# Kernel tuning notes

Hardware: AMD Instinct MI355X
Metric: run time of the kernel (lower is better)

Reference implementation:

```python
import jax, jax.numpy as jnp
import numpy as np

N = 100000         # nodes
E = 800000         # directed edges (before self loops)
F_IN = 64          # num_node_features
HID = 128          # hidden_channels
HEADS = 4
HD = HID // HEADS  # head_dim = 32
NEG_SLOPE = 0.2    # GATv2Conv default negative_slope


def _layernorm(x, g, b, eps=1e-5):
    m = jnp.mean(x, axis=-1, keepdims=True)
    v = jnp.var(x, axis=-1, keepdims=True)
    return (x - m) * jax.lax.rsqrt(v + eps) * g + b


def _gatv2_conv(x, src, dst, w_l, w_r, att, heads, hd):
    # GATv2Conv (share_weights=False, bias=False, concat=True), inference mode.
    n = x.shape[0]
    x_l = (x @ w_l).reshape(n, heads, hd)   # source-side transform
    x_r = (x @ w_r).reshape(n, heads, hd)   # target-side transform
    x_j = x_l[src]                          # [Et, H, C] gather (messages)
    e = jax.nn.leaky_relu(x_j + x_r[dst], NEG_SLOPE)
    logits = jnp.einsum('ehc,hc->eh', e, att)            # [Et, H]
    m = jax.ops.segment_max(logits, dst, num_segments=n)  # stable segment softmax
    p = jnp.exp(logits - m[dst])
    s = jax.ops.segment_sum(p, dst, num_segments=n)
    alpha = p / s[dst]
    out = jax.ops.segment_sum(x_j * alpha[..., None], dst, num_segments=n)
    return out.reshape(n, heads * hd)


def _forward(edge_index, x, ln_in_g, ln_in_b, w_l1, w_r1, att1, ln1_g, ln1_b,
             w_l2, w_r2, att2, ln2_g, ln2_b, w_l3, w_r3, att3, ln3_g, ln3_b,
             rtt_w1, rtt_b1, rtt_w2, rtt_b2, ret_w1, ret_b1, ret_w2, ret_b2):
    n = x.shape[0]
    loops = jnp.arange(n, dtype=edge_index.dtype)
    src = jnp.concatenate([edge_index[0], loops])  # add_self_loops=True
    dst = jnp.concatenate([edge_index[1], loops])
    h = _layernorm(x, ln_in_g, ln_in_b)
    # layer 0: F_IN -> HID (4 heads), no residual (dims differ)
    h = _gatv2_conv(h, src, dst, w_l1, w_r1, att1, HEADS, HD)
    h = jax.nn.relu(_layernorm(h, ln1_g, ln1_b))
    # layer 1: HID -> HID (4 heads), residual * 0.1
    res = h
    h = _gatv2_conv(h, src, dst, w_l2, w_r2, att2, HEADS, HD)
    h = jax.nn.relu(_layernorm(h, ln2_g, ln2_b) + 0.1 * res)
    # layer 2: HID -> HID (1 head), residual * 0.1, no relu (last layer)
    res = h
    h = _gatv2_conv(h, src, dst, w_l3, w_r3, att3, 1, HID)
    h = _layernorm(h, ln3_g, ln3_b) + 0.1 * res
    # prediction heads (dropout inactive at inference)
    rtt = jax.nn.relu(h @ rtt_w1 + rtt_b1) @ rtt_w2 + rtt_b2
    ret = jax.nn.relu(h @ ret_w1 + ret_b1) @ ret_w2 + ret_b2
    return jnp.concatenate([rtt, ret], axis=1)  # [N, 2]


def setup_inputs() -> dict:
    key = jax.random.key(0)
    ks = jax.random.split(key, 32)

    def xavier(k, shape, gain=0.3):
        lim = gain * np.sqrt(6.0 / (shape[0] + shape[1]))
        return jax.random.uniform(k, shape, jnp.float32, -lim, lim)

    inp = {
        'x': jax.random.normal(ks[0], (N, F_IN), jnp.float32),
        'edge_index': jax.random.randint(ks[1], (2, E), 0, N, jnp.int32),
        'ln_in_g': jnp.ones((F_IN,), jnp.float32),
        'ln_in_b': jnp.zeros((F_IN,), jnp.float32),
        'w_l1': xavier(ks[2], (F_IN, HID)),
        'w_r1': xavier(ks[3], (F_IN, HID)),
        'att1': jax.random.normal(ks[4], (HEADS, HD), jnp.float32) * 0.1,
        'ln1_g': jnp.ones((HID,), jnp.float32),
        'ln1_b': jnp.zeros((HID,), jnp.float32),
        'w_l2': xavier(ks[5], (HID, HID)),
        'w_r2': xavier(ks[6], (HID, HID)),
        'att2': jax.random.normal(ks[7], (HEADS, HD), jnp.float32) * 0.1,
        'ln2_g': jnp.ones((HID,), jnp.float32),
        'ln2_b': jnp.zeros((HID,), jnp.float32),
        'w_l3': xavier(ks[8], (HID, HID)),
        'w_r3': xavier(ks[9], (HID, HID)),
        'att3': jax.random.normal(ks[10], (1, HID), jnp.float32) * 0.1,
        'ln3_g': jnp.ones((HID,), jnp.float32),
        'ln3_b': jnp.zeros((HID,), jnp.float32),
        'rtt_w1': xavier(ks[11], (HID, HID // 2)),
        'rtt_b1': jnp.zeros((HID // 2,), jnp.float32),
        'rtt_w2': xavier(ks[12], (HID // 2, 1)),
        'rtt_b2': jnp.zeros((1,), jnp.float32),
        'ret_w1': xavier(ks[13], (HID, HID // 2)),
        'ret_b1': jnp.zeros((HID // 2,), jnp.float32),
        'ret_w2': xavier(ks[14], (HID // 2, 1)),
        'ret_b2': jnp.zeros((1,), jnp.float32),
    }
    return inp


def reference(x, edge_index, ln_in_g, ln_in_b, w_l1, w_r1, att1, ln1_g, ln1_b,
              w_l2, w_r2, att2, ln2_g, ln2_b, w_l3, w_r3, att3, ln3_g, ln3_b,
              rtt_w1, rtt_b1, rtt_w2, rtt_b2, ret_w1, ret_b1, ret_w2, ret_b2):
    return _forward(edge_index, x, ln_in_g, ln_in_b, w_l1, w_r1, att1, ln1_g,
                    ln1_b, w_l2, w_r2, att2, ln2_g, ln2_b, w_l3, w_r3, att3,
                    ln3_g, ln3_b, rtt_w1, rtt_b1, rtt_w2, rtt_b2, ret_w1,
                    ret_b1, ret_w2, ret_b2)
```

## Files before the change

kernel.cpp:

```cpp
#include <hip/hip_runtime.h>
#include <hip/hip_bf16.h>
#include <cstdint>
#include <cstddef>

#define NEG_SLOPE 0.2f

typedef float f4v __attribute__((ext_vector_type(4)));
typedef float f8v __attribute__((ext_vector_type(8)));
typedef _Float16 h8v __attribute__((ext_vector_type(8)));
typedef short short8 __attribute__((ext_vector_type(8)));
typedef float f32x4 __attribute__((ext_vector_type(4)));

__device__ __forceinline__ void cvt2h(float v, _Float16& h, _Float16& l) {
  h = (_Float16)v;
  l = (_Float16)(v - (float)h);
}


__global__ __launch_bounds__(256) void degree_count_kernel(
    const int* __restrict__ ei, int E, int* __restrict__ deg) {
  int e = blockIdx.x * 256 + threadIdx.x;
  if (e < E) atomicAdd(&deg[ei[E + e]], 1);
}

__global__ __launch_bounds__(1024) void scan1_kernel(
    const int* __restrict__ deg, int n, int* __restrict__ incl,
    int* __restrict__ blocksums) {
  __shared__ int sm[1024];
  int t = threadIdx.x;
  int i = blockIdx.x * 1024 + t;
  sm[t] = (i < n) ? (deg[i] + 1) : 0;
  __syncthreads();
  #pragma unroll
  for (int o = 1; o < 1024; o <<= 1) {
    int a = (t >= o) ? sm[t - o] : 0;
    __syncthreads();
    sm[t] += a;
    __syncthreads();
  }
  if (i < n) incl[i] = sm[t];
  if (t == 1023) blocksums[blockIdx.x] = sm[t];
}

__global__ __launch_bounds__(1024) void scan23_kernel(
    const int* __restrict__ incl, const int* __restrict__ deg,
    const int* __restrict__ bs, int nb, int n, int* __restrict__ rowcur) {
  int i = blockIdx.x * 1024 + threadIdx.x;
  if (i >= n) return;
  int off = 0;
  for (int j = 0; j < (int)blockIdx.x; j++) off += bs[j];
  rowcur[i] = incl[i] - (deg[i] + 1) + off;
}

__global__ __launch_bounds__(256) void scatter_kernel(
    const int* __restrict__ ei, int E, int ET, int* __restrict__ rowcur,
    int* __restrict__ csr_src) {
  int e = blockIdx.x * 256 + threadIdx.x;
  if (e >= ET) return;
  int s, d;
  if (e < E) { s = ei[e]; d = ei[E + e]; }
  else       { s = e - E; d = s; }
  int pos = atomicAdd(&rowcur[d], 1);
  csr_src[pos] = s;
}

struct PrepArgs {
  const float* w[8];
  short* o[8];
  int fout[8];
  int cum[9];
};

__global__ __launch_bounds__(256) void prep_w_kernel(PrepArgs pa) {
  int i = blockIdx.x * 256 + threadIdx.x;
  if (i >= pa.cum[8]) return;
  int s = 0;
  while (i >= pa.cum[s + 1]) s++;
  int li = i - pa.cum[s];
  int FOUT = pa.fout[s];
  int NT = FOUT >> 4;
  int sz = pa.cum[s + 1] - pa.cum[s];
  int c = li / (NT * 512);
  int r1 = li % (NT * 512);
  int t = r1 >> 9;
  int e = r1 & 511;
  int lane = e >> 3, j = e & 7;
  int k = c * 32 + (lane >> 4) * 8 + j;
  int n = t * 16 + (lane & 15);
  float v = pa.w[s][k * FOUT + n];
  _Float16 h, l;
  cvt2h(v, h, l);
  pa.o[s][li] = __builtin_bit_cast(short, h);
  pa.o[s][li + sz] = __builtin_bit_cast(short, l);
}

#define MFMA3H(ah, al, bh, bl, acc)                                          \
  acc = __builtin_amdgcn_mfma_f32_16x16x32_f16(ah, bh, acc, 0, 0, 0);       \
  acc = __builtin_amdgcn_mfma_f32_16x16x32_f16(ah, bl, acc, 0, 0, 0);       \
  acc = __builtin_amdgcn_mfma_f32_16x16x32_f16(al, bh, acc, 0, 0, 0);

__global__ __launch_bounds__(256, 4) void mfma_gemm_ln_kernel(
    const float* __restrict__ X, const float* __restrict__ lng,
    const float* __restrict__ lnb, const short* __restrict__ WfL,
    const short* __restrict__ WfR, _Float16* __restrict__ YL,
    float* __restrict__ YR, int nrows) {
  constexpr int NT = 8, TOT = 2 * NT * 512;
  const short* Wf = blockIdx.y ? WfR : WfL;
  const int isL = (blockIdx.y == 0);
  const int wave = threadIdx.x >> 6, lane = threadIdx.x & 63;
  const int quad = lane >> 4, ln16 = lane & 15;
  const int rb = blockIdx.x * 64 + wave * 16;
  int r0 = rb + ln16;
  int rA0 = r0 < nrows ? r0 : nrows - 1;
  const float* xp0 = X + (size_t)rA0 * 64 + quad * 8;

  float av[16];
  *(float4*)&av[0]  = *(const float4*)(xp0);
  *(float4*)&av[4]  = *(const float4*)(xp0 + 4);
  *(float4*)&av[8]  = *(const float4*)(xp0 + 32);
  *(float4*)&av[12] = *(const float4*)(xp0 + 36);

  float s0 = 0.f, q0 = 0.f;
  #pragma unroll
  for (int j = 0; j < 16; j++) {
    s0 += av[j]; q0 += av[j] * av[j];
  }
  s0 += __shfl_xor(s0, 16); s0 += __shfl_xor(s0, 32);
  q0 += __shfl_xor(q0, 16); q0 += __shfl_xor(q0, 32);
  float mean0 = s0 * (1.f / 64.f);
  float rstd0 = rsqrtf(q0 * (1.f / 64.f) - mean0 * mean0 + 1e-5f);

  f32x4 acc[NT];
  #pragma unroll
  for (int t = 0; t < NT; t++) acc[t] = (f32x4){0.f, 0.f, 0.f, 0.f};

  #pragma unroll
  for (int c = 0; c < 2; c++) {
    float4 gv0 = *(const float4*)&lng[quad * 8 + c * 32];
    float4 gv1 = *(const float4*)&lng[quad * 8 + c * 32 + 4];
    float4 bv0 = *(const float4*)&lnb[quad * 8 + c * 32];
    float4 bv1 = *(const float4*)&lnb[quad * 8 + c * 32 + 4];
    float gg[8] = {gv0.x, gv0.y, gv0.z, gv0.w, gv1.x, gv1.y, gv1.z, gv1.w};
    float bb[8] = {bv0.x, bv0.y, bv0.z, bv0.w, bv1.x, bv1.y, bv1.z, bv1.w};
    h8v ah, al;
    #pragma unroll
    for (int j = 0; j < 8; j++) {
      float v0 = (av[c * 8 + j] - mean0) * rstd0 * gg[j] + bb[j];
      _Float16 h, l;
      cvt2h(v0, h, l); ah[j] = h; al[j] = l;
    }
    const short* wp = Wf + c * NT * 512 + lane * 8;
    #pragma unroll
    for (int t = 0; t < NT; t++) {
      h8v bh = *(const h8v*)(wp + t * 512);
      h8v bl = *(const h8v*)(wp + t * 512 + TOT);
      MFMA3H(ah, al, bh, bl, acc[t]);
    }
  }

  const int rbase = rb + quad * 4;
  #pragma unroll
  for (int t = 0; t < NT; t++)
    #pragma unroll
    for (int r = 0; r < 4; r++) {
      int ra = rbase + r;
      if (ra < nrows) {
        if (isL) YL[(size_t)ra * 128 + t * 16 + ln16] = (_Float16)acc[t][r];
        else     YR[(size_t)ra * 128 + t * 16 + ln16] = acc[t][r];
      }
    }
}

__global__ __launch_bounds__(256, 4) void mfma_gemm_lr_kernel(
    const float* __restrict__ X, const short* __restrict__ WfL,
    const short* __restrict__ WfR, _Float16* __restrict__ YL,
    float* __restrict__ YR, int nrows) {
  constexpr int NC = 4, NT = 8, TOT = NC * NT * 512;
  const short* Wf = blockIdx.y ? WfR : WfL;
  const int isL = (blockIdx.y == 0);
  const int wave = threadIdx.x >> 6, lane = threadIdx.x & 63;
  const int quad = lane >> 4, ln16 = lane & 15;
  const int rb = blockIdx.x * 64 + wave * 16;
  int r0 = rb + ln16;
  int rA0 = r0 < nrows ? r0 : nrows - 1;
  const float* xp0 = X + (size_t)rA0 * 128 + quad * 8;

  f32x4 acc[NT];
  #pragma unroll
  for (int t = 0; t < NT; t++) acc[t] = (f32x4){0.f, 0.f, 0.f, 0.f};

  #pragma unroll
  for (int c = 0; c < NC; c++) {
    float4 x00 = *(const float4*)(xp0 + c * 32);
    float4 x01 = *(const float4*)(xp0 + c * 32 + 4);
    float a0[8] = {x00.x, x00.y, x00.z, x00.w, x01.x, x01.y, x01.z, x01.w};
    h8v ah, al;
    #pragma unroll
    for (int j = 0; j < 8; j++) {
      _Float16 h, l;
      cvt2h(a0[j], h, l); ah[j] = h; al[j] = l;
    }
    const short* wp = Wf + c * NT * 512 + lane * 8;
    #pragma unroll
    for (int t = 0; t < NT; t++) {
      h8v bh = *(const h8v*)(wp + t * 512);
      h8v bl = *(const h8v*)(wp + t * 512 + TOT);
      MFMA3H(ah, al, bh, bl, acc[t]);
    }
  }

  const int rbase = rb + quad * 4;
  #pragma unroll
  for (int t = 0; t < NT; t++)
    #pragma unroll
    for (int r = 0; r < 4; r++) {
      int ra = rbase + r;
      if (ra < nrows) {
        if (isL) YL[(size_t)ra * 128 + t * 16 + ln16] = (_Float16)acc[t][r];
        else     YR[(size_t)ra * 128 + t * 16 + ln16] = acc[t][r];
      }
    }
}

__global__ __launch_bounds__(256, 2) void mfma_head_lr_kernel(
    const float* __restrict__ X, const short* __restrict__ Wf1,
    const float* __restrict__ b1a, const float* __restrict__ w2a,
    const float* __restrict__ b2a, const short* __restrict__ Wf2,
    const float* __restrict__ b1b, const float* __restrict__ w2b,
    const float* __restrict__ b2b, float* __restrict__ out, int nrows) {
  constexpr int NC = 4, NT = 4, TOT = NC * NT * 512;
  const int wave = threadIdx.x >> 6, lane = threadIdx.x & 63;
  const int quad = lane >> 4, ln16 = lane & 15;
  int rowA = blockIdx.x * 64 + wave * 16 + ln16;
  int rA = rowA < nrows ? rowA : nrows - 1;
  const float* xp = X + (size_t)rA * 128 + quad * 8;

  f32x4 accL[NT], accR[NT];
  #pragma unroll
  for (int t = 0; t < NT; t++) {
    accL[t] = (f32x4){0.f, 0.f, 0.f, 0.f};
    accR[t] = (f32x4){0.f, 0.f, 0.f, 0.f};
  }

  #pragma unroll
  for (int c = 0; c < NC; c++) {
    float4 a0 = *(const float4*)(xp + c * 32);
    float4 a1 = *(const float4*)(xp + c * 32 + 4);
    float av[8] = {a0.x, a0.y, a0.z, a0.w, a1.x, a1.y, a1.z, a1.w};
    h8v ah, al;
    #pragma unroll
    for (int j = 0; j < 8; j++) {
      _Float16 h, l;
      cvt2h(av[j], h, l);
      ah[j] = h; al[j] = l;
    }
    const short* wpL = Wf1 + c * NT * 512 + lane * 8;
    const short* wpR = Wf2 + c * NT * 512 + lane * 8;
    #pragma unroll
    for (int t = 0; t < NT; t++) {
      h8v bh = *(const h8v*)(wpL + t * 512);
      h8v bl = *(const h8v*)(wpL + t * 512 + TOT);
      MFMA3H(ah, al, bh, bl, accL[t]);
      h8v ch = *(const h8v*)(wpR + t * 512);
      h8v cl = *(const h8v*)(wpR + t * 512 + TOT);
      MFMA3H(ah, al, ch, cl, accR[t]);
    }
  }

  float prA[4] = {0.f, 0.f, 0.f, 0.f};
  float prB[4] = {0.f, 0.f, 0.f, 0.f};
  #pragma unroll
  for (int t = 0; t < NT; t++) {
    float bvA = b1a[t * 16 + ln16], wvA = w2a[t * 16 + ln16];
    float bvB = b1b[t * 16 + ln16], wvB = w2b[t * 16 + ln16];
    #pragma unroll
    for (int r = 0; r < 4; r++) {
      prA[r] += fmaxf(accL[t][r] + bvA, 0.f) * wvA;
      prB[r] += fmaxf(accR[t][r] + bvB, 0.f) * wvB;
    }
  }
  #pragma unroll
  for (int o = 1; o < 16; o <<= 1)
    #pragma unroll
    for (int r = 0; r < 4; r++) {
      prA[r] += __shfl_xor(prA[r], o);
      prB[r] += __shfl_xor(prB[r], o);
    }
  if (ln16 == 0) {
    const float bb2a = b2a[0], bb2b = b2b[0];
    const int rbase = blockIdx.x * 64 + wave * 16 + quad * 4;
    #pragma unroll
    for (int r = 0; r < 4; r++) {
      int rr = rbase + r;
      if (rr < nrows) {
        out[(size_t)rr * 2 + 0] = prA[r] + bb2a;
        out[(size_t)rr * 2 + 1] = prB[r] + bb2b;
      }
    }
  }
}

template <int H>
__global__ __launch_bounds__(64) void gat_fused_kernel(
    const _Float16* __restrict__ xl, const float* __restrict__ xr,
    const int* __restrict__ csr_src, const int* __restrict__ row_end,
    const int* __restrict__ deg, const float* __restrict__ att,
    const float* __restrict__ res, const float* __restrict__ g,
    const float* __restrict__ b, float* __restrict__ y, int n,
    float resScale, int doRelu) {
  int l = threadIdx.x & 63;
  int rh = l >> 5;
  int st = (l >> 4) & 1;
  int ln = l & 15;
  int row = blockIdx.x * 2 + rh;
  int rowC = row < n ? row : n - 1;
  int cb = ln * 32;
  int cbh = ln * 16;
  int end = row_end[rowC];
  int dg = deg[rowC] + 1;
  int start = end - dg;
  int cnt = (dg - st + 1) >> 1;

  const char* xrb = (const char*)xr + (size_t)rowC * 512 + cb;
  f4v xr0 = *(const f4v*)xrb;
  f4v xr1 = *(const f4v*)(xrb + 16);
  f4v av0 = *(const f4v*)((const char*)att + cb);
  f4v av1 = *(const f4v*)((const char*)att + cb + 16);

  float s = 0.f;
  float ac[8] = {0.f, 0.f, 0.f, 0.f, 0.f, 0.f, 0.f, 0.f};

  int idx = start + st;
  h8v pa = (h8v)0, pb = (h8v)0;
  if (cnt > 0)
    pa = *(const h8v*)((const char*)xl + (size_t)csr_src[idx] * 256 + cbh);
  if (cnt > 1)
    pb = *(const h8v*)((const char*)xl + (size_t)csr_src[idx + 2] * 256 + cbh);
  for (int i = 0; i < cnt; i++) {
    f8v xv = __builtin_convertvector(pa, f8v);
    pa = pb;
    if (i + 2 < cnt)
      pb = *(const h8v*)((const char*)xl + (size_t)csr_src[idx + 4] * 256 + cbh);
    idx += 2;
    float p0;
    {
      float t0 = xv[0] + xr0.x, t1 = xv[1] + xr0.y;
      float t2 = xv[2] + xr0.z, t3 = xv[3] + xr0.w;
      float t4 = xv[4] + xr1.x, t5 = xv[5] + xr1.y;
      float t6 = xv[6] + xr1.z, t7 = xv[7] + xr1.w;
      float v0 = fmaxf(t0, NEG_SLOPE * t0), v1 = fmaxf(t1, NEG_SLOPE * t1);
      float v2 = fmaxf(t2, NEG_SLOPE * t2), v3 = fmaxf(t3, NEG_SLOPE * t3);
      float v4 = fmaxf(t4, NEG_SLOPE * t4), v5 = fmaxf(t5, NEG_SLOPE * t5);
      float v6 = fmaxf(t6, NEG_SLOPE * t6), v7 = fmaxf(t7, NEG_SLOPE * t7);
      p0 = v0 * av0.x + v1 * av0.y + v2 * av0.z + v3 * av0.w +
           v4 * av1.x + v5 * av1.y + v6 * av1.z + v7 * av1.w;
    }
    if constexpr (H == 1) {
      #pragma unroll
      for (int o = 1; o < 16; o <<= 1) p0 += __shfl_xor(p0, o);
    } else {
      p0 += __shfl_xor(p0, 1);
      p0 += __shfl_xor(p0, 2);
    }
    float e = __expf(p0);
    s += e;
    ac[0] += e * xv[0]; ac[1] += e * xv[1];
    ac[2] += e * xv[2]; ac[3] += e * xv[3];
    ac[4] += e * xv[4]; ac[5] += e * xv[5];
    ac[6] += e * xv[6]; ac[7] += e * xv[7];
  }
  s += __shfl_xor(s, 16);
  #pragma unroll
  for (int j = 0; j < 8; j++) ac[j] += __shfl_xor(ac[j], 16);

  float inv = 1.f / s;
  float ov[8];
  #pragma unroll
  for (int j = 0; j < 8; j++) ov[j] = ac[j] * inv;

  float sum = 0.f, sq = 0.f;
  #pragma unroll
  for (int j = 0; j < 8; j++) { sum += ov[j]; sq += ov[j] * ov[j]; }
  #pragma unroll
  for (int o = 1; o < 16; o <<= 1) {
    sum += __shfl_xor(sum, o);
    sq += __shfl_xor(sq, o);
  }
  float mean = sum * (1.f / 128.f);
  float var = sq * (1.f / 128.f) - mean * mean;
  float rstd = rsqrtf(var + 1e-5f);

  f4v gv0 = *(const f4v*)((const char*)g + cb);
  f4v gv1 = *(const f4v*)((const char*)g + cb + 16);
  f4v bv0 = *(const f4v*)((const char*)b + cb);
  f4v bv1 = *(const f4v*)((const char*)b + cb + 16);
  float gg[8] = {gv0.x, gv0.y, gv0.z, gv0.w, gv1.x, gv1.y, gv1.z, gv1.w};
  float bb[8] = {bv0.x, bv0.y, bv0.z, bv0.w, bv1.x, bv1.y, bv1.z, bv1.w};
  float rv[8];
  #pragma unroll
  for (int j = 0; j < 8; j++) rv[j] = (ov[j] - mean) * rstd * gg[j] + bb[j];
  if (res) {
    const char* rb = (const char*)res + (size_t)rowC * 512 + cb;
    f4v r0 = *(const f4v*)rb;
    f4v r1 = *(const f4v*)(rb + 16);
    rv[0] += resScale * r0.x; rv[1] += resScale * r0.y;
    rv[2] += resScale * r0.z; rv[3] += resScale * r0.w;
    rv[4] += resScale * r1.x; rv[5] += resScale * r1.y;
    rv[6] += resScale * r1.z; rv[7] += resScale * r1.w;
  }
  if (doRelu) {
    #pragma unroll
    for (int j = 0; j < 8; j++) rv[j] = fmaxf(rv[j], 0.f);
  }
  if (st == 0 && row < n) {
    char* yb = (char*)y + (size_t)row * 512 + cb;
    f4v o0 = {rv[0], rv[1], rv[2], rv[3]};
    f4v o1 = {rv[4], rv[5], rv[6], rv[7]};
    *(f4v*)yb = o0;
    *(f4v*)(yb + 16) = o1;
  }
}

extern "C" void kernel_launch(void* const* d_in, const int* in_sizes, int n_in,
                              void* d_out, int out_size, void* d_ws,
                              size_t ws_size, hipStream_t stream) {
  const float* x       = (const float*)d_in[0];
  const int*   ei      = (const int*)d_in[1];
  const float* ln_in_g = (const float*)d_in[2];
  const float* ln_in_b = (const float*)d_in[3];
  const float* w_l1    = (const float*)d_in[4];
  const float* w_r1    = (const float*)d_in[5];
  const float* att1    = (const float*)d_in[6];
  const float* ln1_g   = (const float*)d_in[7];
  const float* ln1_b   = (const float*)d_in[8];
  const float* w_l2    = (const float*)d_in[9];
  const float* w_r2    = (const float*)d_in[10];
  const float* att2    = (const float*)d_in[11];
  const float* ln2_g   = (const float*)d_in[12];
  const float* ln2_b   = (const float*)d_in[13];
  const float* w_l3    = (const float*)d_in[14];
  const float* w_r3    = (const float*)d_in[15];
  const float* att3    = (const float*)d_in[16];
  const float* ln3_g   = (const float*)d_in[17];
  const float* ln3_b   = (const float*)d_in[18];
  const float* rtt_w1  = (const float*)d_in[19];
  const float* rtt_b1  = (const float*)d_in[20];
  const float* rtt_w2  = (const float*)d_in[21];
  const float* rtt_b2  = (const float*)d_in[22];
  const float* ret_w1  = (const float*)d_in[23];
  const float* ret_b1  = (const float*)d_in[24];
  const float* ret_w2  = (const float*)d_in[25];
  const float* ret_b2  = (const float*)d_in[26];

  const int N = in_sizes[0] / 64;
  const int E = in_sizes[1] / 2;
  const int ET = E + N;
  const size_t NF = (size_t)N * 128;

  float* A = (float*)d_ws;
  _Float16* B = (_Float16*)(A + NF);
  float* C = (float*)(A + 2 * NF);
  int* deg     = (int*)(C + NF);
  int* rowcur  = deg + N;
  int* incl    = rowcur + N;
  int* bsums   = incl + N;
  int* csr_src = bsums + 1024;
  short* wf = (short*)(((uintptr_t)(csr_src + ET) + 63) & ~(uintptr_t)63);

  float* out = (float*)d_out;

  const int segsz[8] = {64 * 128, 64 * 128, 128 * 128, 128 * 128,
                        128 * 128, 128 * 128, 128 * 64, 128 * 64};
  PrepArgs pa;
  pa.w[0] = w_l1; pa.w[1] = w_r1; pa.w[2] = w_l2; pa.w[3] = w_r2;
  pa.w[4] = w_l3; pa.w[5] = w_r3; pa.w[6] = rtt_w1; pa.w[7] = ret_w1;
  pa.fout[0] = 128; pa.fout[1] = 128; pa.fout[2] = 128; pa.fout[3] = 128;
  pa.fout[4] = 128; pa.fout[5] = 128; pa.fout[6] = 64; pa.fout[7] = 64;
  int acc = 0;
  short* op = wf;
  for (int s = 0; s < 8; s++) {
    pa.cum[s] = acc;
    pa.o[s] = op;
    op += 2 * segsz[s];
    acc += segsz[s];
  }
  pa.cum[8] = acc;

  const int mmBlocks   = (N + 63) / 64;
  const int gatBlocks  = (N + 1) / 2;
  const int NB = (N + 1023) / 1024;
  dim3 lrGrid(mmBlocks, 2);

  prep_w_kernel<<<(acc + 255) / 256, 256, 0, stream>>>(pa);

  hipMemsetAsync(deg, 0, (size_t)N * sizeof(int), stream);
  degree_count_kernel<<<(E + 255) / 256, 256, 0, stream>>>(ei, E, deg);
  scan1_kernel<<<NB, 1024, 0, stream>>>(deg, N, incl, bsums);
  scan23_kernel<<<NB, 1024, 0, stream>>>(incl, deg, bsums, NB, N, rowcur);
  scatter_kernel<<<(ET + 255) / 256, 256, 0, stream>>>(ei, E, ET, rowcur, csr_src);

  mfma_gemm_ln_kernel<<<lrGrid, 256, 0, stream>>>(
      x, ln_in_g, ln_in_b, pa.o[0], pa.o[1], B, C, N);
  gat_fused_kernel<4><<<gatBlocks, 64, 0, stream>>>(
      B, C, csr_src, rowcur, deg, att1, nullptr, ln1_g, ln1_b, A, N, 0.f, 1);

  mfma_gemm_lr_kernel<<<lrGrid, 256, 0, stream>>>(A, pa.o[2], pa.o[3], B, C, N);
  gat_fused_kernel<4><<<gatBlocks, 64, 0, stream>>>(
      B, C, csr_src, rowcur, deg, att2, A, ln2_g, ln2_b, A, N, 0.1f, 1);

  mfma_gemm_lr_kernel<<<lrGrid, 256, 0, stream>>>(A, pa.o[4], pa.o[5], B, C, N);
  gat_fused_kernel<1><<<gatBlocks, 64, 0, stream>>>(
      B, C, csr_src, rowcur, deg, att3, A, ln3_g, ln3_b, A, N, 0.1f, 0);

  mfma_head_lr_kernel<<<mmBlocks, 256, 0, stream>>>(
      A, pa.o[6], rtt_b1, rtt_w2, rtt_b2, pa.o[7], ret_b1, ret_w2, ret_b2,
      out, N);
}
```

Baseline: 533.4 us.

## Store intermediate activations and x_r in fp16, drop split-precision activation MFMA

Switches the workspace buffers for layer outputs, residuals and the target-side transform x_r from fp32 to fp16, halving their memory traffic in the GEMM and the fused GAT kernels. Because activations are now already fp16, the GEMMs load them directly and drop the low-part activation MFMA, using two MFMAs per tile instead of three. This trades precision, since activations and x_r lose the hi/lo split accuracy, for less bandwidth and compute.

```diff
diff --git a/kernel.cpp b/kernel.cpp
--- a/kernel.cpp
+++ b/kernel.cpp
@@ -8,7 +8,6 @@
 typedef float f4v __attribute__((ext_vector_type(4)));
 typedef float f8v __attribute__((ext_vector_type(8)));
 typedef _Float16 h8v __attribute__((ext_vector_type(8)));
-typedef short short8 __attribute__((ext_vector_type(8)));
 typedef float f32x4 __attribute__((ext_vector_type(4)));
 
 __device__ __forceinline__ void cvt2h(float v, _Float16& h, _Float16& l) {
@@ -99,14 +98,18 @@
   acc = __builtin_amdgcn_mfma_f32_16x16x32_f16(ah, bl, acc, 0, 0, 0);       \
   acc = __builtin_amdgcn_mfma_f32_16x16x32_f16(al, bh, acc, 0, 0, 0);
 
+#define MFMA2H(ah, bh, bl, acc)                                              \
+  acc = __builtin_amdgcn_mfma_f32_16x16x32_f16(ah, bh, acc, 0, 0, 0);       \
+  acc = __builtin_amdgcn_mfma_f32_16x16x32_f16(ah, bl, acc, 0, 0, 0);
+
 __global__ __launch_bounds__(256, 4) void mfma_gemm_ln_kernel(
     const float* __restrict__ X, const float* __restrict__ lng,
     const float* __restrict__ lnb, const short* __restrict__ WfL,
     const short* __restrict__ WfR, _Float16* __restrict__ YL,
-    float* __restrict__ YR, int nrows) {
+    _Float16* __restrict__ YR, int nrows) {
   constexpr int NT = 8, TOT = 2 * NT * 512;
   const short* Wf = blockIdx.y ? WfR : WfL;
-  const int isL = (blockIdx.y == 0);
+  _Float16* Y = blockIdx.y ? YR : YL;
   const int wave = threadIdx.x >> 6, lane = threadIdx.x & 63;
   const int quad = lane >> 4, ln16 = lane & 15;
   const int rb = blockIdx.x * 64 + wave * 16;
@@ -164,26 +167,23 @@
     #pragma unroll
     for (int r = 0; r < 4; r++) {
       int ra = rbase + r;
-      if (ra < nrows) {
-        if (isL) YL[(size_t)ra * 128 + t * 16 + ln16] = (_Float16)acc[t][r];
-        else     YR[(size_t)ra * 128 + t * 16 + ln16] = acc[t][r];
-      }
+      if (ra < nrows) Y[(size_t)ra * 128 + t * 16 + ln16] = (_Float16)acc[t][r];
     }
 }
 
 __global__ __launch_bounds__(256, 4) void mfma_gemm_lr_kernel(
-    const float* __restrict__ X, const short* __restrict__ WfL,
+    const _Float16* __restrict__ X, const short* __restrict__ WfL,
     const short* __restrict__ WfR, _Float16* __restrict__ YL,
-    float* __restrict__ YR, int nrows) {
+    _Float16* __restrict__ YR, int nrows) {
   constexpr int NC = 4, NT = 8, TOT = NC * NT * 512;
   const short* Wf = blockIdx.y ? WfR : WfL;
-  const int isL = (blockIdx.y == 0);
+  _Float16* Y = blockIdx.y ? YR : YL;
   const int wave = threadIdx.x >> 6, lane = threadIdx.x & 63;
   const int quad = lane >> 4, ln16 = lane & 15;
   const int rb = blockIdx.x * 64 + wave * 16;
   int r0 = rb + ln16;
   int rA0 = r0 < nrows ? r0 : nrows - 1;
-  const float* xp0 = X + (size_t)rA0 * 128 + quad * 8;
+  const _Float16* xp0 = X + (size_t)rA0 * 128 + quad * 8;
 
   f32x4 acc[NT];
   #pragma unroll
@@ -191,21 +191,13 @@
 
   #pragma unroll
   for (int c = 0; c < NC; c++) {
-    float4 x00 = *(const float4*)(xp0 + c * 32);
-    float4 x01 = *(const float4*)(xp0 + c * 32 + 4);
-    float a0[8] = {x00.x, x00.y, x00.z, x00.w, x01.x, x01.y, x01.z, x01.w};
-    h8v ah, al;
-    #pragma unroll
-    for (int j = 0; j < 8; j++) {
-      _Float16 h, l;
-      cvt2h(a0[j], h, l); ah[j] = h; al[j] = l;
-    }
+    h8v ah = *(const h8v*)(xp0 + c * 32);
     const short* wp = Wf + c * NT * 512 + lane * 8;
     #pragma unroll
     for (int t = 0; t < NT; t++) {
       h8v bh = *(const h8v*)(wp + t * 512);
       h8v bl = *(const h8v*)(wp + t * 512 + TOT);
-      MFMA3H(ah, al, bh, bl, acc[t]);
+      MFMA2H(ah, bh, bl, acc[t]);
     }
   }
 
@@ -215,15 +207,12 @@
     #pragma unroll
     for (int r = 0; r < 4; r++) {
       int ra = rbase + r;
-      if (ra < nrows) {
-        if (isL) YL[(size_t)ra * 128 + t * 16 + ln16] = (_Float16)acc[t][r];
-        else     YR[(size_t)ra * 128 + t * 16 + ln16] = acc[t][r];
-      }
+      if (ra < nrows) Y[(size_t)ra * 128 + t * 16 + ln16] = (_Float16)acc[t][r];
     }
 }
 
 __global__ __launch_bounds__(256, 2) void mfma_head_lr_kernel(
-    const float* __restrict__ X, const short* __restrict__ Wf1,
+    const _Float16* __restrict__ X, const short* __restrict__ Wf1,
     const float* __restrict__ b1a, const float* __restrict__ w2a,
     const float* __restrict__ b2a, const short* __restrict__ Wf2,
     const float* __restrict__ b1b, const float* __restrict__ w2b,
@@ -233,7 +222,7 @@
   const int quad = lane >> 4, ln16 = lane & 15;
   int rowA = blockIdx.x * 64 + wave * 16 + ln16;
   int rA = rowA < nrows ? rowA : nrows - 1;
-  const float* xp = X + (size_t)rA * 128 + quad * 8;
+  const _Float16* xp = X + (size_t)rA * 128 + quad * 8;
 
   f32x4 accL[NT], accR[NT];
   #pragma unroll
@@ -244,26 +233,17 @@
 
   #pragma unroll
   for (int c = 0; c < NC; c++) {
-    float4 a0 = *(const float4*)(xp + c * 32);
-    float4 a1 = *(const float4*)(xp + c * 32 + 4);
-    float av[8] = {a0.x, a0.y, a0.z, a0.w, a1.x, a1.y, a1.z, a1.w};
-    h8v ah, al;
-    #pragma unroll
-    for (int j = 0; j < 8; j++) {
-      _Float16 h, l;
-      cvt2h(av[j], h, l);
-      ah[j] = h; al[j] = l;
-    }
+    h8v ah = *(const h8v*)(xp + c * 32);
     const short* wpL = Wf1 + c * NT * 512 + lane * 8;
     const short* wpR = Wf2 + c * NT * 512 + lane * 8;
     #pragma unroll
     for (int t = 0; t < NT; t++) {
       h8v bh = *(const h8v*)(wpL + t * 512);
       h8v bl = *(const h8v*)(wpL + t * 512 + TOT);
-      MFMA3H(ah, al, bh, bl, accL[t]);
+      MFMA2H(ah, bh, bl, accL[t]);
       h8v ch = *(const h8v*)(wpR + t * 512);
       h8v cl = *(const h8v*)(wpR + t * 512 + TOT);
-      MFMA3H(ah, al, ch, cl, accR[t]);
+      MFMA2H(ah, ch, cl, accR[t]);
     }
   }
 
@@ -302,11 +282,11 @@
 
 template <int H>
 __global__ __launch_bounds__(64) void gat_fused_kernel(
-    const _Float16* __restrict__ xl, const float* __restrict__ xr,
+    const _Float16* __restrict__ xl, const _Float16* __restrict__ xr,
     const int* __restrict__ csr_src, const int* __restrict__ row_end,
     const int* __restrict__ deg, const float* __restrict__ att,
-    const float* __restrict__ res, const float* __restrict__ g,
-    const float* __restrict__ b, float* __restrict__ y, int n,
+    const _Float16* __restrict__ res, const float* __restrict__ g,
+    const float* __restrict__ b, _Float16* __restrict__ y, int n,
     float resScale, int doRelu) {
   int l = threadIdx.x & 63;
   int rh = l >> 5;
@@ -321,9 +301,8 @@
   int start = end - dg;
   int cnt = (dg - st + 1) >> 1;
 
-  const char* xrb = (const char*)xr + (size_t)rowC * 512 + cb;
-  f4v xr0 = *(const f4v*)xrb;
-  f4v xr1 = *(const f4v*)(xrb + 16);
+  h8v xrh = *(const h8v*)((const char*)xr + (size_t)rowC * 256 + cbh);
+  f8v xrf = __builtin_convertvector(xrh, f8v);
   f4v av0 = *(const f4v*)((const char*)att + cb);
   f4v av1 = *(const f4v*)((const char*)att + cb + 16);
 
@@ -344,10 +323,10 @@
     idx += 2;
     float p0;
     {
-      float t0 = xv[0] + xr0.x, t1 = xv[1] + xr0.y;
-      float t2 = xv[2] + xr0.z, t3 = xv[3] + xr0.w;
-      float t4 = xv[4] + xr1.x, t5 = xv[5] + xr1.y;
-      float t6 = xv[6] + xr1.z, t7 = xv[7] + xr1.w;
+      float t0 = xv[0] + xrf[0], t1 = xv[1] + xrf[1];
+      float t2 = xv[2] + xrf[2], t3 = xv[3] + xrf[3];
+      float t4 = xv[4] + xrf[4], t5 = xv[5] + xrf[5];
+      float t6 = xv[6] + xrf[6], t7 = xv[7] + xrf[7];
       float v0 = fmaxf(t0, NEG_SLOPE * t0), v1 = fmaxf(t1, NEG_SLOPE * t1);
       float v2 = fmaxf(t2, NEG_SLOPE * t2), v3 = fmaxf(t3, NEG_SLOPE * t3);
       float v4 = fmaxf(t4, NEG_SLOPE * t4), v5 = fmaxf(t5, NEG_SLOPE * t5);
@@ -400,24 +379,21 @@
   #pragma unroll
   for (int j = 0; j < 8; j++) rv[j] = (ov[j] - mean) * rstd * gg[j] + bb[j];
   if (res) {
-    const char* rb = (const char*)res + (size_t)rowC * 512 + cb;
-    f4v r0 = *(const f4v*)rb;
-    f4v r1 = *(const f4v*)(rb + 16);
-    rv[0] += resScale * r0.x; rv[1] += resScale * r0.y;
-    rv[2] += resScale * r0.z; rv[3] += resScale * r0.w;
-    rv[4] += resScale * r1.x; rv[5] += resScale * r1.y;
-    rv[6] += resScale * r1.z; rv[7] += resScale * r1.w;
+    h8v rr = *(const h8v*)((const char*)res + (size_t)rowC * 256 + cbh);
+    f8v rf = __builtin_convertvector(rr, f8v);
+    #pragma unroll
+    for (int j = 0; j < 8; j++) rv[j] += resScale * rf[j];
   }
   if (doRelu) {
     #pragma unroll
     for (int j = 0; j < 8; j++) rv[j] = fmaxf(rv[j], 0.f);
   }
   if (st == 0 && row < n) {
-    char* yb = (char*)y + (size_t)row * 512 + cb;
-    f4v o0 = {rv[0], rv[1], rv[2], rv[3]};
-    f4v o1 = {rv[4], rv[5], rv[6], rv[7]};
-    *(f4v*)yb = o0;
-    *(f4v*)(yb + 16) = o1;
+    f8v of;
+    #pragma unroll
+    for (int j = 0; j < 8; j++) of[j] = rv[j];
+    h8v oh = __builtin_convertvector(of, h8v);
+    *(h8v*)((char*)y + (size_t)row * 256 + cbh) = oh;
   }
 }
 
@@ -457,9 +433,9 @@
   const int ET = E + N;
   const size_t NF = (size_t)N * 128;
 
-  float* A = (float*)d_ws;
-  _Float16* B = (_Float16*)(A + NF);
-  float* C = (float*)(A + 2 * NF);
+  _Float16* A = (_Float16*)d_ws;
+  _Float16* B = A + NF;
+  _Float16* C = B + NF;
   int* deg     = (int*)(C + NF);
   int* rowcur  = deg + N;
   int* incl    = rowcur + N;
```

Measured after the change: 503.5 us. 1.06x faster.
